# Kernel optimization log

Hardware: AMD Instinct MI355X
Metric: run time of the kernel (lower is better)

The kernel has to match this reference:

```python
import jax, jax.numpy as jnp
import numpy as np

ATTN_MASK_VALUE = -1e10
N, D_IN, D_HEAD, D_OUT = 8192, 1024, 128, 1024


def setup_inputs() -> dict:
    key = jax.random.key(0)
    k_x, k_wqkv, k_bqkv, k_wo, k_bo = jax.random.split(key, 5)
    x = jax.random.normal(k_x, (N, D_IN), dtype=jnp.float32)
    # flax Dense default: lecun_normal kernel, zeros bias; use scaled normal for test
    w_qkv = jax.random.normal(k_wqkv, (D_IN, 3 * D_HEAD), dtype=jnp.float32) / np.sqrt(D_IN)
    b_qkv = jnp.zeros((3 * D_HEAD,), dtype=jnp.float32)
    w_out = jax.random.normal(k_wo, (D_HEAD, D_OUT), dtype=jnp.float32) / np.sqrt(D_HEAD)
    b_out = jnp.zeros((D_OUT,), dtype=jnp.float32)
    return {"x": x, "w_qkv": w_qkv, "b_qkv": b_qkv, "w_out": w_out, "b_out": b_out}


def reference(x, w_qkv, b_qkv, w_out, b_out):
    n = x.shape[0]
    scale = D_HEAD ** (-0.5)
    qkv = x @ w_qkv + b_qkv                      # [n, 3*dh]
    q, k, v = jnp.split(qkv, 3, axis=-1)         # each [n, dh]
    sim = jnp.einsum('id,jd->ij', q, k) * scale  # [n, n]
    mask = jnp.triu(jnp.ones((n, n), dtype=bool), 1)
    sim = jnp.where(mask, ATTN_MASK_VALUE, sim)
    attn = jax.nn.softmax(sim, axis=-1)
    out = jnp.einsum('ij,jd->id', attn, v)       # [n, dh]
    return out @ w_out + b_out                   # [n, d_out]
```

## Files before the change

kernel.cpp:

```cpp
#include <hip/hip_runtime.h>
#include <stdint.h>

typedef __attribute__((ext_vector_type(4))) float f32x4;
typedef __attribute__((ext_vector_type(8))) __bf16 bf16x8;

#define MFMA16(a, b, c) __builtin_amdgcn_mfma_f32_16x16x32_bf16(a, b, c, 0, 0, 0)
#define GLOAD16(g, l)                                                              \
  __builtin_amdgcn_global_load_lds(                                                \
      (const __attribute__((address_space(1))) unsigned int*)(g),                  \
      (__attribute__((address_space(3))) unsigned int*)(l), 16, 0, 0)
#define EXP2F(x) __builtin_amdgcn_exp2f(x)

static __device__ __forceinline__ unsigned short f2b(float f) {
  unsigned int u = __float_as_uint(f);
  u += 0x7fff + ((u >> 16) & 1);
  return (unsigned short)(u >> 16);
}

#define NROWS 8192
#define DIN   1024
#define DH    128
#define DOUT  1024

__global__ void k_convert_w(const float* __restrict__ wqkv, const float* __restrict__ wout,
                            unsigned short* __restrict__ wqkvT, unsigned short* __restrict__ woutT) {
  __shared__ float t[64][65];
  const int bid = blockIdx.x;
  const float* src;
  unsigned short* dst;
  int k0, n0, sstride, dstride;
  if (bid < 96) {
    int kt = bid / 6, nt = bid % 6;
    k0 = kt * 64; n0 = nt * 64;
    src = wqkv; sstride = 384; dst = wqkvT; dstride = 1024;
  } else {
    int b2 = bid - 96;
    int kt = b2 & 1, nt = b2 >> 1;
    k0 = kt * 64; n0 = nt * 64;
    src = wout; sstride = 1024; dst = woutT; dstride = 128;
  }
  const int tid = threadIdx.x;
  const int r = tid >> 4, c4 = (tid & 15) * 4;
#pragma unroll
  for (int j = 0; j < 4; ++j) {
    int rr = r + j * 16;
    float4 v = *reinterpret_cast<const float4*>(src + (size_t)(k0 + rr) * sstride + n0 + c4);
    t[rr][c4 + 0] = v.x; t[rr][c4 + 1] = v.y; t[rr][c4 + 2] = v.z; t[rr][c4 + 3] = v.w;
  }
  __syncthreads();
#pragma unroll
  for (int j = 0; j < 4; ++j) {
    int rn = r + j * 16;
    ushort4 h;
    h.x = f2b(t[c4 + 0][rn]); h.y = f2b(t[c4 + 1][rn]);
    h.z = f2b(t[c4 + 2][rn]); h.w = f2b(t[c4 + 3][rn]);
    *reinterpret_cast<ushort4*>(dst + (size_t)(n0 + rn) * dstride + k0 + c4) = h;
  }
}

__global__ void k_convert_x(const float* __restrict__ x, unsigned short* __restrict__ xb) {
  int i = (blockIdx.x * 256 + threadIdx.x) * 4;
  float4 v = *reinterpret_cast<const float4*>(x + i);
  ushort4 h;
  h.x = f2b(v.x); h.y = f2b(v.y); h.z = f2b(v.z); h.w = f2b(v.w);
  *reinterpret_cast<ushort4*>(xb + i) = h;
}

__launch_bounds__(256, 2)
__global__ void k_qkv_gemm(const unsigned short* __restrict__ xb, const unsigned short* __restrict__ wT,
                           const float* __restrict__ bqkv,
                           unsigned short* __restrict__ Qb, unsigned short* __restrict__ Kb,
                           unsigned short* __restrict__ Vb) {
  const int hb = blockIdx.x;
  const int xcd = hb & 7, jj = hb >> 3;
  const int tau = xcd * 24 + jj;
  const int bn = tau % 3, bm = tau / 3;
  const int tid = threadIdx.x;
  const int lane = tid & 63, w = tid >> 6;
  const int l15 = lane & 15, g = lane >> 4;
  const int wm = (w >> 1) * 64, wn = (w & 1) * 64;
  const int row0 = bm * 128, col0 = bn * 128;

  __shared__ __align__(16) char Ash[2][16384];
  __shared__ __align__(16) char Bsh[2][16384];

  f32x4 acc[4][4] = {};

#define QKV_STAGE(k0, buf)                                                          \
  {                                                                                 \
    _Pragma("unroll")                                                               \
    for (int j2 = 0; j2 < 4; ++j2) {                                                \
      int idx = j2 * 256 + tid;                                                     \
      int r = idx >> 3, gg = idx & 7, sgg = gg ^ (r & 7);                           \
      GLOAD16(xb + (size_t)(row0 + r) * DIN + (k0) + sgg * 8, Ash[buf] + idx * 16); \
      GLOAD16(wT + (size_t)(col0 + r) * DIN + (k0) + sgg * 8, Bsh[buf] + idx * 16); \
    }                                                                               \
  }

  QKV_STAGE(0, 0);
  __syncthreads();
  int cur = 0;
  for (int k0 = 0; k0 < DIN; k0 += 64) {
    if (k0 + 64 < DIN) QKV_STAGE(k0 + 64, cur ^ 1);
#pragma unroll
    for (int ksl = 0; ksl < 2; ++ksl) {
      bf16x8 af[4], bfr[4];
#pragma unroll
      for (int i = 0; i < 4; ++i) {
        int r = wm + i * 16 + l15;
        int ba = r * 128 + ksl * 64 + g * 16;
        af[i] = *reinterpret_cast<bf16x8*>(Ash[cur] + (ba ^ ((r & 7) << 4)));
        int n = wn + i * 16 + l15;
        int bb = n * 128 + ksl * 64 + g * 16;
        bfr[i] = *reinterpret_cast<bf16x8*>(Bsh[cur] + (bb ^ ((n & 7) << 4)));
      }
#pragma unroll
      for (int i = 0; i < 4; ++i)
#pragma unroll
        for (int jn = 0; jn < 4; ++jn)
          acc[i][jn] = MFMA16(af[i], bfr[jn], acc[i][jn]);
    }
    __syncthreads();
    cur ^= 1;
  }

  unsigned short* outb = (bn == 0) ? Qb : (bn == 1 ? Kb : Vb);
#pragma unroll
  for (int i = 0; i < 4; ++i)
#pragma unroll
    for (int jn = 0; jn < 4; ++jn)
#pragma unroll
      for (int r = 0; r < 4; ++r) {
        int grow = row0 + wm + i * 16 + g * 4 + r;
        int lcol = wn + jn * 16 + l15;
        float vv = acc[i][jn][r] + bqkv[bn * 128 + lcol];
        outb[(size_t)grow * DH + lcol] = f2b(vv);
      }
}

__global__ void k_transpose_v(const unsigned short* __restrict__ V, unsigned short* __restrict__ VT) {
  __shared__ __align__(16) unsigned short t[64 * 128];
  const int b = blockIdx.x;
  const int tid = threadIdx.x;
  const int kv0 = b * 64;
#pragma unroll
  for (int j = 0; j < 4; ++j) {
    int c = j * 256 + tid;
    int r = c >> 4, cc = (c & 15) * 8;
    uint4 v = *reinterpret_cast<const uint4*>(V + (size_t)(kv0 + r) * DH + cc);
    int col = (cc + ((r >> 3) & 7) * 8) & 127;
    *reinterpret_cast<uint4*>(&t[r * 128 + col]) = v;
  }
  __syncthreads();
#pragma unroll
  for (int j = 0; j < 4; ++j) {
    int c = j * 256 + tid;
    int d = c >> 3, kk = (c & 7) * 8;
    unsigned short tmp[8];
#pragma unroll
    for (int e = 0; e < 8; ++e) {
      int r = kk + e;
      int col = (d + ((r >> 3) & 7) * 8) & 127;
      tmp[e] = t[r * 128 + col];
    }
    *reinterpret_cast<uint4*>(VT + (size_t)d * NROWS + kv0 + kk) = *reinterpret_cast<uint4*>(tmp);
  }
}

__launch_bounds__(256, 2)
__global__ void k_flash(const unsigned short* __restrict__ Q, const unsigned short* __restrict__ Kg,
                        const unsigned short* __restrict__ VT,
                        float* __restrict__ Opart, float* __restrict__ MLpart, int LQ) {
  const int ci = blockIdx.x;
  const int t = (int)(gridDim.y - 1) - (int)blockIdx.y;
  const int Jq = 1 << LQ;
  if (ci * Jq > t) return;
  const int qb = t << 7;
  const int ks = ci * (Jq << 7);
  const int ke = min(ks + (Jq << 7), qb + 128);
  const int nsteps = (ke - ks) >> 6;

  const int a = t >> LQ, b = t & (Jq - 1);
  const int slot = t + ((Jq * a * (a - 1)) >> 1) + a * b + ci;

  const int tid = threadIdx.x;
  const int lane = tid & 63, w = tid >> 6;
  const int l15 = lane & 15, g = lane >> 4;

  __shared__ __align__(16) char Ksh[2][16384];
  __shared__ __align__(16) char Vsh[2][16384];
  __shared__ __align__(16) char Psh[4][4096];

  const int qr0 = qb + w * 16 + l15;
  const int qr1 = qr0 + 64;
  bf16x8 qf0[4], qf1[4];
#pragma unroll
  for (int d = 0; d < 4; ++d) {
    qf0[d] = *reinterpret_cast<const bf16x8*>(Q + (size_t)qr0 * DH + d * 32 + g * 8);
    qf1[d] = *reinterpret_cast<const bf16x8*>(Q + (size_t)qr1 * DH + d * 32 + g * 8);
  }

  f32x4 acco0[8] = {}, acco1[8] = {};
  float m0 = -1e30f, l0 = 0.f, m1 = -1e30f, l1 = 0.f;
  const float c2 = 0.08838834764831843f * 1.4426950408889634f;

#define FL_STAGE(kv0, buf)                                                            \
  {                                                                                   \
    _Pragma("unroll")                                                                 \
    for (int j2 = 0; j2 < 4; ++j2) {                                                  \
      int idx = j2 * 256 + tid;                                                       \
      int r = idx >> 4, gg = idx & 15, sgg = gg ^ (r & 7);                            \
      GLOAD16(Kg + (size_t)((kv0) + r) * DH + sgg * 8, Ksh[buf] + idx * 16);          \
    }                                                                                 \
    _Pragma("unroll")                                                                 \
    for (int j2 = 0; j2 < 4; ++j2) {                                                  \
      int idx = j2 * 256 + tid;                                                       \
      int d = idx >> 3, gg = idx & 7, sgg = gg ^ (d & 7);                             \
      GLOAD16(VT + (size_t)d * NROWS + (kv0) + sgg * 8, Vsh[buf] + idx * 16);         \
    }                                                                                 \
  }

  char* Pw = Psh[w];

  FL_STAGE(ks, 0);
  __syncthreads();
  int cur = 0;

  for (int s = 0; s < nsteps; ++s) {
    const int kv0 = ks + (s << 6);
    if (s + 1 < nsteps) FL_STAGE(kv0 + 64, cur ^ 1);
    const bool act0 = (kv0 < qb + 64);

    f32x4 accs0[4] = {}, accs1[4] = {};
    if (act0) {
#pragma unroll
      for (int jc = 0; jc < 4; ++jc)
#pragma unroll
        for (int d = 0; d < 4; ++d) {
          int r = jc * 16 + l15;
          int byte = r * 256 + d * 64 + g * 16; byte ^= (r & 7) << 4;
          bf16x8 kf = *reinterpret_cast<bf16x8*>(Ksh[cur] + byte);
          accs1[jc] = MFMA16(kf, qf1[d], accs1[jc]);
          accs0[jc] = MFMA16(kf, qf0[d], accs0[jc]);
        }
    } else {
#pragma unroll
      for (int jc = 0; jc < 4; ++jc)
#pragma unroll
        for (int d = 0; d < 4; ++d) {
          int r = jc * 16 + l15;
          int byte = r * 256 + d * 64 + g * 16; byte ^= (r & 7) << 4;
          bf16x8 kf = *reinterpret_cast<bf16x8*>(Ksh[cur] + byte);
          accs1[jc] = MFMA16(kf, qf1[d], accs1[jc]);
        }
    }

#define SOFTMAX_PW(ACCS, ACCO, M, L, QROW, ROWBASE)                                   \
    {                                                                                 \
      float p[4][4];                                                                  \
      float mx = -3e38f;                                                              \
      _Pragma("unroll")                                                               \
      for (int jc = 0; jc < 4; ++jc)                                                  \
        _Pragma("unroll")                                                             \
        for (int r = 0; r < 4; ++r) {                                                 \
          float sv = ACCS[jc][r] * c2;                                                \
          int kk = kv0 + jc * 16 + (g << 2) + r;                                      \
          sv = (kk <= (QROW)) ? sv : -3e38f;                                          \
          p[jc][r] = sv;                                                              \
          mx = fmaxf(mx, sv);                                                         \
        }                                                                             \
      mx = fmaxf(mx, __shfl_xor(mx, 16));                                             \
      mx = fmaxf(mx, __shfl_xor(mx, 32));                                             \
      float mnew = fmaxf(M, mx);                                                      \
      float fac = EXP2F(M - mnew);                                                    \
      float ps = 0.f;                                                                 \
      _Pragma("unroll")                                                               \
      for (int jc = 0; jc < 4; ++jc)                                                  \
        _Pragma("unroll")                                                             \
        for (int r = 0; r < 4; ++r) {                                                 \
          float e = EXP2F(p[jc][r] - mnew);                                           \
          p[jc][r] = e; ps += e;                                                      \
        }                                                                             \
      ps += __shfl_xor(ps, 16);                                                       \
      ps += __shfl_xor(ps, 32);                                                       \
      L = L * fac + ps;                                                               \
      M = mnew;                                                                       \
      _Pragma("unroll")                                                               \
      for (int dc = 0; dc < 8; ++dc)                                                  \
        _Pragma("unroll")                                                             \
        for (int r = 0; r < 4; ++r) ACCO[dc][r] *= fac;                               \
      int rq = (ROWBASE) + l15;                                                       \
      _Pragma("unroll")                                                               \
      for (int jc = 0; jc < 4; ++jc) {                                                \
        ushort4 pb;                                                                   \
        pb.x = f2b(p[jc][0]); pb.y = f2b(p[jc][1]);                                   \
        pb.z = f2b(p[jc][2]); pb.w = f2b(p[jc][3]);                                   \
        int byte = rq * 128 + jc * 32 + g * 8; byte ^= (rq & 7) << 4;                 \
        *reinterpret_cast<ushort4*>(Pw + byte) = pb;                                  \
      }                                                                               \
    }

    if (act0) SOFTMAX_PW(accs0, acco0, m0, l0, qr0, 0);
    SOFTMAX_PW(accs1, acco1, m1, l1, qr1, 16);
    __asm__ volatile("s_waitcnt lgkmcnt(0)" ::: "memory");
    __builtin_amdgcn_sched_barrier(0);

    bf16x8 pf1[2];
#pragma unroll
    for (int ks2 = 0; ks2 < 2; ++ks2) {
      int rq = 16 + l15;
      int byte = rq * 128 + ks2 * 64 + g * 16; byte ^= (rq & 7) << 4;
      pf1[ks2] = *reinterpret_cast<bf16x8*>(Pw + byte);
    }
    if (act0) {
      bf16x8 pf0[2];
#pragma unroll
      for (int ks2 = 0; ks2 < 2; ++ks2) {
        int byte = l15 * 128 + ks2 * 64 + g * 16; byte ^= (l15 & 7) << 4;
        pf0[ks2] = *reinterpret_cast<bf16x8*>(Pw + byte);
      }
#pragma unroll
      for (int dc = 0; dc < 8; ++dc) {
        int vr = dc * 16 + l15;
        int b0 = vr * 128 + g * 16; b0 ^= (vr & 7) << 4;
        bf16x8 vf0 = *reinterpret_cast<bf16x8*>(Vsh[cur] + b0);
        bf16x8 vf1 = *reinterpret_cast<bf16x8*>(Vsh[cur] + (b0 ^ 64));
        acco1[dc] = MFMA16(vf0, pf1[0], acco1[dc]);
        acco1[dc] = MFMA16(vf1, pf1[1], acco1[dc]);
        acco0[dc] = MFMA16(vf0, pf0[0], acco0[dc]);
        acco0[dc] = MFMA16(vf1, pf0[1], acco0[dc]);
      }
    } else {
#pragma unroll
      for (int dc = 0; dc < 8; ++dc) {
        int vr = dc * 16 + l15;
        int b0 = vr * 128 + g * 16; b0 ^= (vr & 7) << 4;
        bf16x8 vf0 = *reinterpret_cast<bf16x8*>(Vsh[cur] + b0);
        bf16x8 vf1 = *reinterpret_cast<bf16x8*>(Vsh[cur] + (b0 ^ 64));
        acco1[dc] = MFMA16(vf0, pf1[0], acco1[dc]);
        acco1[dc] = MFMA16(vf1, pf1[1], acco1[dc]);
      }
    }
    __syncthreads();
    cur ^= 1;
  }

  const size_t r0 = (size_t)slot * 128 + w * 16 + l15;
  const size_t r1 = r0 + 64;
#pragma unroll
  for (int dc = 0; dc < 8; ++dc) {
    f32x4 o0, o1;
#pragma unroll
    for (int r = 0; r < 4; ++r) { o0[r] = acco0[dc][r]; o1[r] = acco1[dc][r]; }
    *reinterpret_cast<f32x4*>(Opart + r0 * DH + dc * 16 + (g << 2)) = o0;
    *reinterpret_cast<f32x4*>(Opart + r1 * DH + dc * 16 + (g << 2)) = o1;
  }
  if (g == 0) {
    MLpart[r0 * 2 + 0] = m0;
    MLpart[r0 * 2 + 1] = l0;
    MLpart[r1 * 2 + 0] = m1;
    MLpart[r1 * 2 + 1] = l1;
  }
}

__global__ void k_merge(const float* __restrict__ Opart, const float* __restrict__ MLpart,
                        unsigned short* __restrict__ O, int LQ) {
  int tg = blockIdx.x * 256 + threadIdx.x;
  int row = tg >> 5, d4 = (tg & 31) * 4;
  int t = row >> 7;
  int Jq = 1 << LQ;
  int a = t >> LQ, b = t & (Jq - 1);
  int base = t + ((Jq * a * (a - 1)) >> 1) + a * b;
  int nc = a + 1;
  int rowin = row & 127;
  float M = -3e38f;
  for (int i = 0; i < nc; ++i) M = fmaxf(M, MLpart[((size_t)(base + i) * 128 + rowin) * 2]);
  float L = 0.f;
  f32x4 acc = {};
  for (int i = 0; i < nc; ++i) {
    size_t sr = (size_t)(base + i) * 128 + rowin;
    float mi = MLpart[sr * 2];
    float li = MLpart[sr * 2 + 1];
    float wg = EXP2F(mi - M);
    L += li * wg;
    f32x4 o = *reinterpret_cast<const f32x4*>(Opart + sr * DH + d4);
#pragma unroll
    for (int e = 0; e < 4; ++e) acc[e] += wg * o[e];
  }
  float inv = 1.f / L;
  ushort4 hv;
  hv.x = f2b(acc[0] * inv); hv.y = f2b(acc[1] * inv);
  hv.z = f2b(acc[2] * inv); hv.w = f2b(acc[3] * inv);
  *reinterpret_cast<ushort4*>(O + (size_t)row * DH + d4) = hv;
}

__launch_bounds__(256, 2)
__global__ void k_out_gemm(const unsigned short* __restrict__ O, const unsigned short* __restrict__ wT,
                           const float* __restrict__ bout, float* __restrict__ out) {
  const int hb = blockIdx.x;
  const int xcd = hb & 7, jj = hb >> 3;
  const int tau = xcd * 256 + jj;
  const int bn = tau & 15, bm = tau >> 4;
  const int tid = threadIdx.x;
  const int lane = tid & 63, w = tid >> 6;
  const int l15 = lane & 15, g = lane >> 4;
  const int wm = (w >> 1) * 32, wn = (w & 1) * 32;
  const int row0 = bm * 64, col0 = bn * 64;

  __shared__ __align__(16) char Ash[16384];
  __shared__ __align__(16) char Bsh[16384];

#pragma unroll
  for (int j = 0; j < 4; ++j) {
    int idx = j * 256 + tid;
    int r = idx >> 4, gg = idx & 15;
    int sgg = gg ^ (r & 7);
    GLOAD16(O + (size_t)(row0 + r) * DH + sgg * 8, Ash + idx * 16);
    GLOAD16(wT + (size_t)(col0 + r) * DH + sgg * 8, Bsh + idx * 16);
  }
  __syncthreads();

  f32x4 acc[2][2] = {};
#pragma unroll
  for (int ksl = 0; ksl < 4; ++ksl) {
    bf16x8 af[2], bfr[2];
#pragma unroll
    for (int i = 0; i < 2; ++i) {
      int r = wm + i * 16 + l15;
      int ba = r * 256 + ksl * 64 + g * 16;
      af[i] = *reinterpret_cast<bf16x8*>(Ash + (ba ^ ((r & 7) << 4)));
      int n = wn + i * 16 + l15;
      int bb = n * 256 + ksl * 64 + g * 16;
      bfr[i] = *reinterpret_cast<bf16x8*>(Bsh + (bb ^ ((n & 7) << 4)));
    }
#pragma unroll
    for (int i = 0; i < 2; ++i)
#pragma unroll
      for (int jn = 0; jn < 2; ++jn)
        acc[i][jn] = MFMA16(af[i], bfr[jn], acc[i][jn]);
  }

#pragma unroll
  for (int i = 0; i < 2; ++i)
#pragma unroll
    for (int jn = 0; jn < 2; ++jn)
#pragma unroll
      for (int r = 0; r < 4; ++r) {
        int grow = row0 + wm + i * 16 + g * 4 + r;
        int gcol = col0 + wn + jn * 16 + l15;
        out[(size_t)grow * DOUT + gcol] = acc[i][jn][r] + bout[gcol];
      }
}

extern "C" void kernel_launch(void* const* d_in, const int* in_sizes, int n_in,
                              void* d_out, int out_size, void* d_ws, size_t ws_size,
                              hipStream_t stream) {
  const float* x    = (const float*)d_in[0];
  const float* wqkv = (const float*)d_in[1];
  const float* bqkv = (const float*)d_in[2];
  const float* wout = (const float*)d_in[3];
  const float* bout = (const float*)d_in[4];
  float* out = (float*)d_out;

  size_t fixed = 786432 + 262144 + (size_t)NROWS * DIN * 2 + (size_t)5 * NROWS * DH * 2;
  int LQ = 2;
  size_t slots = 0;
  for (; LQ <= 6; ++LQ) {
    int Jq = 1 << LQ, A = 64 / Jq;
    slots = (size_t)Jq * A * (A + 1) / 2;
    size_t need = fixed + slots * ((size_t)128 * DH * 4 + 128 * 8);
    if (need <= ws_size || LQ == 6) break;
  }

  char* ws = (char*)d_ws;
  size_t off = 0;
  unsigned short* wqkvT = (unsigned short*)(ws + off); off += (size_t)384 * 1024 * 2;
  unsigned short* woutT = (unsigned short*)(ws + off); off += (size_t)1024 * 128 * 2;
  unsigned short* xb  = (unsigned short*)(ws + off); off += (size_t)NROWS * DIN * 2;
  unsigned short* Qb  = (unsigned short*)(ws + off); off += (size_t)NROWS * DH * 2;
  unsigned short* Kb  = (unsigned short*)(ws + off); off += (size_t)NROWS * DH * 2;
  unsigned short* Vb  = (unsigned short*)(ws + off); off += (size_t)NROWS * DH * 2;
  unsigned short* VTb = (unsigned short*)(ws + off); off += (size_t)NROWS * DH * 2;
  unsigned short* Ob  = (unsigned short*)(ws + off); off += (size_t)NROWS * DH * 2;
  float* Opart  = (float*)(ws + off); off += slots * (size_t)128 * DH * 4;
  float* MLpart = (float*)(ws + off); off += slots * (size_t)128 * 8;

  k_convert_w<<<128, 256, 0, stream>>>(wqkv, wout, wqkvT, woutT);
  k_convert_x<<<(NROWS * DIN) / 1024, 256, 0, stream>>>(x, xb);
  k_qkv_gemm<<<192, 256, 0, stream>>>(xb, wqkvT, bqkv, Qb, Kb, Vb);
  k_transpose_v<<<128, 256, 0, stream>>>(Vb, VTb);
  k_flash<<<dim3(64 >> LQ, 64), 256, 0, stream>>>(Qb, Kb, VTb, Opart, MLpart, LQ);
  k_merge<<<(NROWS * 32) / 256, 256, 0, stream>>>(Opart, MLpart, Ob, LQ);
  k_out_gemm<<<2048, 256, 0, stream>>>(Ob, woutT, bout, out);
}
```

Baseline: 115.9 us.

## Retile QKV and output GEMMs, store flash partials in bf16, add MFMA priority hints

The QKV GEMM moves to 128x64 tiles and 384 blocks so the 256-CU device gets more blocks than the previous 192. The output GEMM moves from 64x64 single-shot tiles to 128x128 tiles with a double-buffered K loop over 512 blocks. Flash partial outputs are stored as bf16 instead of fp32, which halves partial-buffer traffic in the flash and merge kernels at some cost in precision. s_setprio is raised around the MFMA sections of the flash kernel to favour matrix-core issue.

```diff
diff --git a/kernel.cpp b/kernel.cpp
--- a/kernel.cpp
+++ b/kernel.cpp
@@ -15,6 +15,10 @@
   unsigned int u = __float_as_uint(f);
   u += 0x7fff + ((u >> 16) & 1);
   return (unsigned short)(u >> 16);
+}
+static __device__ __forceinline__ float b2f(unsigned short h) {
+  unsigned int u = ((unsigned int)h) << 16;
+  return __uint_as_float(u);
 }
 
 #define NROWS 8192
@@ -73,18 +77,18 @@
                            unsigned short* __restrict__ Vb) {
   const int hb = blockIdx.x;
   const int xcd = hb & 7, jj = hb >> 3;
-  const int tau = xcd * 24 + jj;
-  const int bn = tau % 3, bm = tau / 3;
+  const int tau = xcd * 48 + jj;
+  const int bn = tau % 6, bm = tau / 6;
   const int tid = threadIdx.x;
   const int lane = tid & 63, w = tid >> 6;
   const int l15 = lane & 15, g = lane >> 4;
-  const int wm = (w >> 1) * 64, wn = (w & 1) * 64;
-  const int row0 = bm * 128, col0 = bn * 128;
+  const int wm = (w >> 1) * 64, wn = (w & 1) * 32;
+  const int row0 = bm * 128, col0 = bn * 64;
 
   __shared__ __align__(16) char Ash[2][16384];
-  __shared__ __align__(16) char Bsh[2][16384];
-
-  f32x4 acc[4][4] = {};
+  __shared__ __align__(16) char Bsh[2][8192];
+
+  f32x4 acc[4][2] = {};
 
 #define QKV_STAGE(k0, buf)                                                          \
   {                                                                                 \
@@ -93,6 +97,11 @@
       int idx = j2 * 256 + tid;                                                     \
       int r = idx >> 3, gg = idx & 7, sgg = gg ^ (r & 7);                           \
       GLOAD16(xb + (size_t)(row0 + r) * DIN + (k0) + sgg * 8, Ash[buf] + idx * 16); \
+    }                                                                               \
+    _Pragma("unroll")                                                               \
+    for (int j2 = 0; j2 < 2; ++j2) {                                                \
+      int idx = j2 * 256 + tid;                                                     \
+      int r = idx >> 3, gg = idx & 7, sgg = gg ^ (r & 7);                           \
       GLOAD16(wT + (size_t)(col0 + r) * DIN + (k0) + sgg * 8, Bsh[buf] + idx * 16); \
     }                                                                               \
   }
@@ -104,37 +113,42 @@
     if (k0 + 64 < DIN) QKV_STAGE(k0 + 64, cur ^ 1);
 #pragma unroll
     for (int ksl = 0; ksl < 2; ++ksl) {
-      bf16x8 af[4], bfr[4];
+      bf16x8 af[4], bfr[2];
 #pragma unroll
       for (int i = 0; i < 4; ++i) {
         int r = wm + i * 16 + l15;
         int ba = r * 128 + ksl * 64 + g * 16;
         af[i] = *reinterpret_cast<bf16x8*>(Ash[cur] + (ba ^ ((r & 7) << 4)));
-        int n = wn + i * 16 + l15;
+      }
+#pragma unroll
+      for (int jn = 0; jn < 2; ++jn) {
+        int n = wn + jn * 16 + l15;
         int bb = n * 128 + ksl * 64 + g * 16;
-        bfr[i] = *reinterpret_cast<bf16x8*>(Bsh[cur] + (bb ^ ((n & 7) << 4)));
+        bfr[jn] = *reinterpret_cast<bf16x8*>(Bsh[cur] + (bb ^ ((n & 7) << 4)));
       }
 #pragma unroll
       for (int i = 0; i < 4; ++i)
 #pragma unroll
-        for (int jn = 0; jn < 4; ++jn)
+        for (int jn = 0; jn < 2; ++jn)
           acc[i][jn] = MFMA16(af[i], bfr[jn], acc[i][jn]);
     }
     __syncthreads();
     cur ^= 1;
   }
 
-  unsigned short* outb = (bn == 0) ? Qb : (bn == 1 ? Kb : Vb);
+  const int which = col0 >> 7;
+  const int inner = col0 & 127;
+  unsigned short* outb = (which == 0) ? Qb : (which == 1 ? Kb : Vb);
 #pragma unroll
   for (int i = 0; i < 4; ++i)
 #pragma unroll
-    for (int jn = 0; jn < 4; ++jn)
+    for (int jn = 0; jn < 2; ++jn)
 #pragma unroll
       for (int r = 0; r < 4; ++r) {
         int grow = row0 + wm + i * 16 + g * 4 + r;
         int lcol = wn + jn * 16 + l15;
-        float vv = acc[i][jn][r] + bqkv[bn * 128 + lcol];
-        outb[(size_t)grow * DH + lcol] = f2b(vv);
+        float vv = acc[i][jn][r] + bqkv[col0 + lcol];
+        outb[(size_t)grow * DH + inner + lcol] = f2b(vv);
       }
 }
 
@@ -170,7 +184,7 @@
 __launch_bounds__(256, 2)
 __global__ void k_flash(const unsigned short* __restrict__ Q, const unsigned short* __restrict__ Kg,
                         const unsigned short* __restrict__ VT,
-                        float* __restrict__ Opart, float* __restrict__ MLpart, int LQ) {
+                        unsigned short* __restrict__ Opart, float* __restrict__ MLpart, int LQ) {
   const int ci = blockIdx.x;
   const int t = (int)(gridDim.y - 1) - (int)blockIdx.y;
   const int Jq = 1 << LQ;
@@ -232,6 +246,7 @@
     const bool act0 = (kv0 < qb + 64);
 
     f32x4 accs0[4] = {}, accs1[4] = {};
+    __builtin_amdgcn_s_setprio(1);
     if (act0) {
 #pragma unroll
       for (int jc = 0; jc < 4; ++jc)
@@ -254,6 +269,7 @@
           accs1[jc] = MFMA16(kf, qf1[d], accs1[jc]);
         }
     }
+    __builtin_amdgcn_s_setprio(0);
 
 #define SOFTMAX_PW(ACCS, ACCO, M, L, QROW, ROWBASE)                                   \
     {                                                                                 \
@@ -312,6 +328,7 @@
       int byte = rq * 128 + ks2 * 64 + g * 16; byte ^= (rq & 7) << 4;
       pf1[ks2] = *reinterpret_cast<bf16x8*>(Pw + byte);
     }
+    __builtin_amdgcn_s_setprio(1);
     if (act0) {
       bf16x8 pf0[2];
 #pragma unroll
@@ -341,6 +358,7 @@
         acco1[dc] = MFMA16(vf1, pf1[1], acco1[dc]);
       }
     }
+    __builtin_amdgcn_s_setprio(0);
     __syncthreads();
     cur ^= 1;
   }
@@ -349,11 +367,13 @@
   const size_t r1 = r0 + 64;
 #pragma unroll
   for (int dc = 0; dc < 8; ++dc) {
-    f32x4 o0, o1;
-#pragma unroll
-    for (int r = 0; r < 4; ++r) { o0[r] = acco0[dc][r]; o1[r] = acco1[dc][r]; }
-    *reinterpret_cast<f32x4*>(Opart + r0 * DH + dc * 16 + (g << 2)) = o0;
-    *reinterpret_cast<f32x4*>(Opart + r1 * DH + dc * 16 + (g << 2)) = o1;
+    ushort4 o0, o1;
+    o0.x = f2b(acco0[dc][0]); o0.y = f2b(acco0[dc][1]);
+    o0.z = f2b(acco0[dc][2]); o0.w = f2b(acco0[dc][3]);
+    o1.x = f2b(acco1[dc][0]); o1.y = f2b(acco1[dc][1]);
+    o1.z = f2b(acco1[dc][2]); o1.w = f2b(acco1[dc][3]);
+    *reinterpret_cast<ushort4*>(Opart + r0 * DH + dc * 16 + (g << 2)) = o0;
+    *reinterpret_cast<ushort4*>(Opart + r1 * DH + dc * 16 + (g << 2)) = o1;
   }
   if (g == 0) {
     MLpart[r0 * 2 + 0] = m0;
@@ -363,7 +383,7 @@
   }
 }
 
-__global__ void k_merge(const float* __restrict__ Opart, const float* __restrict__ MLpart,
+__global__ void k_merge(const unsigned short* __restrict__ Opart, const float* __restrict__ MLpart,
                         unsigned short* __restrict__ O, int LQ) {
   int tg = blockIdx.x * 256 + threadIdx.x;
   int row = tg >> 5, d4 = (tg & 31) * 4;
@@ -383,9 +403,9 @@
     float li = MLpart[sr * 2 + 1];
     float wg = EXP2F(mi - M);
     L += li * wg;
-    f32x4 o = *reinterpret_cast<const f32x4*>(Opart + sr * DH + d4);
-#pragma unroll
-    for (int e = 0; e < 4; ++e) acc[e] += wg * o[e];
+    ushort4 o = *reinterpret_cast<const ushort4*>(Opart + sr * DH + d4);
+    acc[0] += wg * b2f(o.x); acc[1] += wg * b2f(o.y);
+    acc[2] += wg * b2f(o.z); acc[3] += wg * b2f(o.w);
   }
   float inv = 1.f / L;
   ushort4 hv;
@@ -399,51 +419,61 @@
                            const float* __restrict__ bout, float* __restrict__ out) {
   const int hb = blockIdx.x;
   const int xcd = hb & 7, jj = hb >> 3;
-  const int tau = xcd * 256 + jj;
-  const int bn = tau & 15, bm = tau >> 4;
+  const int tau = xcd * 64 + jj;
+  const int bn = tau & 7, bm = tau >> 3;
   const int tid = threadIdx.x;
   const int lane = tid & 63, w = tid >> 6;
   const int l15 = lane & 15, g = lane >> 4;
-  const int wm = (w >> 1) * 32, wn = (w & 1) * 32;
-  const int row0 = bm * 64, col0 = bn * 64;
-
-  __shared__ __align__(16) char Ash[16384];
-  __shared__ __align__(16) char Bsh[16384];
-
-#pragma unroll
-  for (int j = 0; j < 4; ++j) {
-    int idx = j * 256 + tid;
-    int r = idx >> 4, gg = idx & 15;
-    int sgg = gg ^ (r & 7);
-    GLOAD16(O + (size_t)(row0 + r) * DH + sgg * 8, Ash + idx * 16);
-    GLOAD16(wT + (size_t)(col0 + r) * DH + sgg * 8, Bsh + idx * 16);
-  }
+  const int wm = (w >> 1) * 64, wn = (w & 1) * 64;
+  const int row0 = bm * 128, col0 = bn * 128;
+
+  __shared__ __align__(16) char Ash[2][16384];
+  __shared__ __align__(16) char Bsh[2][16384];
+
+  f32x4 acc[4][4] = {};
+
+#define OUT_STAGE(k0, buf)                                                          \
+  {                                                                                 \
+    _Pragma("unroll")                                                               \
+    for (int j2 = 0; j2 < 4; ++j2) {                                                \
+      int idx = j2 * 256 + tid;                                                     \
+      int r = idx >> 3, gg = idx & 7, sgg = gg ^ (r & 7);                           \
+      GLOAD16(O + (size_t)(row0 + r) * DH + (k0) + sgg * 8, Ash[buf] + idx * 16);   \
+      GLOAD16(wT + (size_t)(col0 + r) * DH + (k0) + sgg * 8, Bsh[buf] + idx * 16);  \
+    }                                                                               \
+  }
+
+  OUT_STAGE(0, 0);
   __syncthreads();
-
-  f32x4 acc[2][2] = {};
-#pragma unroll
-  for (int ksl = 0; ksl < 4; ++ksl) {
-    bf16x8 af[2], bfr[2];
-#pragma unroll
-    for (int i = 0; i < 2; ++i) {
-      int r = wm + i * 16 + l15;
-      int ba = r * 256 + ksl * 64 + g * 16;
-      af[i] = *reinterpret_cast<bf16x8*>(Ash + (ba ^ ((r & 7) << 4)));
-      int n = wn + i * 16 + l15;
-      int bb = n * 256 + ksl * 64 + g * 16;
-      bfr[i] = *reinterpret_cast<bf16x8*>(Bsh + (bb ^ ((n & 7) << 4)));
-    }
-#pragma unroll
-    for (int i = 0; i < 2; ++i)
-#pragma unroll
-      for (int jn = 0; jn < 2; ++jn)
-        acc[i][jn] = MFMA16(af[i], bfr[jn], acc[i][jn]);
-  }
-
-#pragma unroll
-  for (int i = 0; i < 2; ++i)
-#pragma unroll
-    for (int jn = 0; jn < 2; ++jn)
+  int cur = 0;
+  for (int k0 = 0; k0 < DH; k0 += 64) {
+    if (k0 + 64 < DH) OUT_STAGE(k0 + 64, cur ^ 1);
+#pragma unroll
+    for (int ksl = 0; ksl < 2; ++ksl) {
+      bf16x8 af[4], bfr[4];
+#pragma unroll
+      for (int i = 0; i < 4; ++i) {
+        int r = wm + i * 16 + l15;
+        int ba = r * 128 + ksl * 64 + g * 16;
+        af[i] = *reinterpret_cast<bf16x8*>(Ash[cur] + (ba ^ ((r & 7) << 4)));
+        int n = wn + i * 16 + l15;
+        int bb = n * 128 + ksl * 64 + g * 16;
+        bfr[i] = *reinterpret_cast<bf16x8*>(Bsh[cur] + (bb ^ ((n & 7) << 4)));
+      }
+#pragma unroll
+      for (int i = 0; i < 4; ++i)
+#pragma unroll
+        for (int jn = 0; jn < 4; ++jn)
+          acc[i][jn] = MFMA16(af[i], bfr[jn], acc[i][jn]);
+    }
+    __syncthreads();
+    cur ^= 1;
+  }
+
+#pragma unroll
+  for (int i = 0; i < 4; ++i)
+#pragma unroll
+    for (int jn = 0; jn < 4; ++jn)
 #pragma unroll
       for (int r = 0; r < 4; ++r) {
         int grow = row0 + wm + i * 16 + g * 4 + r;
@@ -468,7 +498,7 @@
   for (; LQ <= 6; ++LQ) {
     int Jq = 1 << LQ, A = 64 / Jq;
     slots = (size_t)Jq * A * (A + 1) / 2;
-    size_t need = fixed + slots * ((size_t)128 * DH * 4 + 128 * 8);
+    size_t need = fixed + slots * ((size_t)128 * DH * 2 + 128 * 8);
     if (need <= ws_size || LQ == 6) break;
   }
 
@@ -482,14 +512,14 @@
   unsigned short* Vb  = (unsigned short*)(ws + off); off += (size_t)NROWS * DH * 2;
   unsigned short* VTb = (unsigned short*)(ws + off); off += (size_t)NROWS * DH * 2;
   unsigned short* Ob  = (unsigned short*)(ws + off); off += (size_t)NROWS * DH * 2;
-  float* Opart  = (float*)(ws + off); off += slots * (size_t)128 * DH * 4;
+  unsigned short* Opart = (unsigned short*)(ws + off); off += slots * (size_t)128 * DH * 2;
   float* MLpart = (float*)(ws + off); off += slots * (size_t)128 * 8;
 
   k_convert_w<<<128, 256, 0, stream>>>(wqkv, wout, wqkvT, woutT);
   k_convert_x<<<(NROWS * DIN) / 1024, 256, 0, stream>>>(x, xb);
-  k_qkv_gemm<<<192, 256, 0, stream>>>(xb, wqkvT, bqkv, Qb, Kb, Vb);
+  k_qkv_gemm<<<384, 256, 0, stream>>>(xb, wqkvT, bqkv, Qb, Kb, Vb);
   k_transpose_v<<<128, 256, 0, stream>>>(Vb, VTb);
   k_flash<<<dim3(64 >> LQ, 64), 256, 0, stream>>>(Qb, Kb, VTb, Opart, MLpart, LQ);
   k_merge<<<(NROWS * 32) / 256, 256, 0, stream>>>(Opart, MLpart, Ob, LQ);
-  k_out_gemm<<<2048, 256, 0, stream>>>(Ob, woutT, bout, out);
-}
+  k_out_gemm<<<512, 256, 0, stream>>>(Ob, woutT, bout, out);
+}
```

New measurement: 115.5 us. No clear change (-0.4%).
